# Optimization experiments

Measured on AMD Instinct MI355X. Metric: run time of the kernel, lower is better.

## Reference

```python
import jax, jax.numpy as jnp
import numpy as np

NUM_HEADS = 16

def setup_inputs() -> dict:
    key = jax.random.key(0)
    k1, k2, k3 = jax.random.split(key, 3)
    B, S, H = 2, 2048, 1024
    x = jax.random.normal(k1, (B, S, H), dtype=jnp.float32)
    w_qkv = jax.random.normal(k2, (H, 3 * H), dtype=jnp.float32) * (1.0 / np.sqrt(H))
    w_out = jax.random.normal(k3, (H, H), dtype=jnp.float32) * (1.0 / np.sqrt(H))
    return {"x": x, "w_qkv": w_qkv, "w_out": w_out}

def reference(x, w_qkv, w_out):
    B, S, H = x.shape
    nh = NUM_HEADS
    dh = H // nh
    qkv = x @ w_qkv  # (B, S, 3H)
    q, k, v = jnp.split(qkv, 3, axis=-1)
    # (B, nh, S, dh)
    q = q.reshape(B, S, nh, dh).transpose(0, 2, 1, 3)
    k = k.reshape(B, S, nh, dh).transpose(0, 2, 1, 3)
    v = v.reshape(B, S, nh, dh).transpose(0, 2, 1, 3)
    att = jnp.einsum('bhsd,bhSd->bhsS', q, k) / np.sqrt(dh).astype(np.float32)
    causal = jnp.tril(jnp.ones((S, S), dtype=bool))
    att = jnp.where(causal[None, None], att, -jnp.inf)
    att = jax.nn.softmax(att, axis=-1)
    out = jnp.einsum('bhsS,bhSd->bhsd', att, v)
    out = out.transpose(0, 2, 1, 3).reshape(B, S, H)
    return out @ w_out
```

## Files before the change

### kernel.cpp

```cpp
#include <hip/hip_runtime.h>

#define DEVINL __device__ __forceinline__

typedef __attribute__((ext_vector_type(8)))  __bf16         bf16x8;
typedef __attribute__((ext_vector_type(4)))  float          f32x4;
typedef __attribute__((ext_vector_type(16))) float          f32x16;
typedef __attribute__((ext_vector_type(8)))  unsigned short ushort8;
typedef __attribute__((ext_vector_type(4)))  unsigned short ushort4v;
typedef __attribute__((ext_vector_type(4)))  unsigned int   uint4v;
typedef __attribute__((ext_vector_type(4)))  float          float4v;

DEVINL unsigned short f2bf(float f) {
  unsigned int u = __float_as_uint(f);
  u += 0x7fffu + ((u >> 16) & 1u);
  return (unsigned short)(u >> 16);
}

DEVINL bf16x8 ldbf8(const unsigned short* p) {
  return __builtin_bit_cast(bf16x8, *(const ushort8*)p);
}

DEVINL unsigned cvtpk_bf16(float lo, float hi) {
  unsigned r;
  asm("v_cvt_pk_bf16_f32 %0, %1, %2" : "=v"(r) : "v"(lo), "v"(hi));
  return r;
}

DEVINL void gload_lds16(const unsigned short* g, unsigned short* l) {
  __builtin_amdgcn_global_load_lds((const __attribute__((address_space(1))) void*)g,
                                   (__attribute__((address_space(3))) void*)l, 16, 0, 0);
}

__global__ __launch_bounds__(256) void cvt_f32_bf16_kernel(
    const float* __restrict__ in, unsigned short* __restrict__ out, int n4) {
  int i = blockIdx.x * 256 + threadIdx.x;
  const int stride = gridDim.x * 256;
  for (; i < n4; i += stride) {
    float4v v = *(const float4v*)(in + (size_t)4 * i);
    ushort4v o;
    o[0] = f2bf(v[0]); o[1] = f2bf(v[1]); o[2] = f2bf(v[2]); o[3] = f2bf(v[3]);
    *(ushort4v*)(out + (size_t)4 * i) = o;
  }
}

__global__ __launch_bounds__(256) void transpose_cvt_kernel(
    const float* __restrict__ in, unsigned short* __restrict__ out, int R, int C) {
  __shared__ float tile[32][33];
  const int tx = threadIdx.x & 31, ty = threadIdx.x >> 5;
  const int r0 = blockIdx.y << 5, c0 = blockIdx.x << 5;
#pragma unroll
  for (int i = 0; i < 32; i += 8)
    tile[ty + i][tx] = in[(size_t)(r0 + ty + i) * C + (c0 + tx)];
  __syncthreads();
#pragma unroll
  for (int i = 0; i < 32; i += 8)
    out[(size_t)(c0 + ty + i) * R + (r0 + tx)] = f2bf(tile[tx][ty + i]);
}

__global__ __launch_bounds__(256) void v_transpose_kernel(
    const unsigned short* __restrict__ qkv, unsigned short* __restrict__ VtG) {
  const int S = 2048, LD = 3072;
  const int s0 = blockIdx.x << 5;
  const int bh = blockIdx.y;
  const int b = bh >> 4, h = bh & 15;
  __shared__ __align__(16) unsigned short T[32][72];
  const int t = threadIdx.x;
  {
    const int s = t >> 3, d0 = (t & 7) << 3;
    *(ushort8*)&T[s][d0] =
        *(const ushort8*)(qkv + ((size_t)(b * S) + s0 + s) * LD + 2048 + h * 64 + d0);
  }
  __syncthreads();
  {
    const int d = t >> 2, sc = (t & 3) << 3;
    ushort8 o;
#pragma unroll
    for (int e = 0; e < 8; ++e) o[e] = T[sc + e][d];
    *(ushort8*)(VtG + ((size_t)bh * 64 + d) * S + s0 + sc) = o;
  }
}

template <bool OUT_BF16>
__global__ __launch_bounds__(256, 3) void gemm_bt_kernel(
    const unsigned short* __restrict__ A,
    const unsigned short* __restrict__ Bt,
    void* __restrict__ Cout,
    int M, int N, int K, int lda, int ldb, int ldc) {
  __shared__ __align__(16) unsigned short As[2][128 * 32];
  __shared__ __align__(16) unsigned short Bs[2][128 * 32];
  const int tid = threadIdx.x;
  const int lane = tid & 63, wave = tid >> 6;
  const int wr = wave >> 1, wc = wave & 1;
  const int g = lane >> 4, q = lane & 15;
  const int row0 = blockIdx.x << 7, col0 = blockIdx.y << 7;

  const int srow = tid >> 2;
  const int sg = ((tid & 3) ^ (srow & 3)) << 3;
  const unsigned short* Ap0 = A + (size_t)(row0 + srow) * lda + sg;
  const unsigned short* Ap1 = Ap0 + (size_t)64 * lda;
  const unsigned short* Bp0 = Bt + (size_t)(col0 + srow) * ldb + sg;
  const unsigned short* Bp1 = Bp0 + (size_t)64 * ldb;

  f32x4 acc[4][4] = {};

  gload_lds16(Ap0, &As[0][wave * 512]);
  gload_lds16(Ap1, &As[0][2048 + wave * 512]);
  gload_lds16(Bp0, &Bs[0][wave * 512]);
  gload_lds16(Bp1, &Bs[0][2048 + wave * 512]);

  const int gx = (g ^ (q & 3)) << 3;
  const int nk = K >> 5;
  int cur = 0;

  for (int t = 0; t < nk; ++t) {
    if (t + 1 < nk) {
      Ap0 += 32; Ap1 += 32; Bp0 += 32; Bp1 += 32;
      gload_lds16(Ap0, &As[cur ^ 1][wave * 512]);
      gload_lds16(Ap1, &As[cur ^ 1][2048 + wave * 512]);
      gload_lds16(Bp0, &Bs[cur ^ 1][wave * 512]);
      gload_lds16(Bp1, &Bs[cur ^ 1][2048 + wave * 512]);
      asm volatile("s_waitcnt vmcnt(4)" ::: "memory");
    } else {
      asm volatile("s_waitcnt vmcnt(0)" ::: "memory");
    }
    __builtin_amdgcn_s_barrier();

    bf16x8 af[4], bfr[4];
#pragma unroll
    for (int mb = 0; mb < 4; ++mb)
      af[mb] = ldbf8(&As[cur][(wr * 64 + mb * 16 + q) * 32] + gx);
#pragma unroll
    for (int nb = 0; nb < 4; ++nb)
      bfr[nb] = ldbf8(&Bs[cur][(wc * 64 + nb * 16 + q) * 32] + gx);
#pragma unroll
    for (int mb = 0; mb < 4; ++mb)
#pragma unroll
      for (int nb = 0; nb < 4; ++nb)
        acc[mb][nb] = __builtin_amdgcn_mfma_f32_16x16x32_bf16(af[mb], bfr[nb], acc[mb][nb], 0, 0, 0);

    __builtin_amdgcn_s_barrier();
    cur ^= 1;
  }

#pragma unroll
  for (int mb = 0; mb < 4; ++mb)
#pragma unroll
    for (int nb = 0; nb < 4; ++nb)
#pragma unroll
      for (int r = 0; r < 4; ++r) {
        const int row = row0 + wr * 64 + mb * 16 + g * 4 + r;
        const int col = col0 + wc * 64 + nb * 16 + q;
        const float v = acc[mb][nb][r];
        if (OUT_BF16) ((unsigned short*)Cout)[(size_t)row * ldc + col] = f2bf(v);
        else          ((float*)Cout)[(size_t)row * ldc + col] = v;
      }
}

__global__ __launch_bounds__(256, 2) void attn_kernel(
    const unsigned short* __restrict__ qkv,
    const unsigned short* __restrict__ VtG,
    unsigned short* __restrict__ O) {
  const int S = 2048, H = 1024, LD = 3072;
  const int wave = threadIdx.x >> 6, lane = threadIdx.x & 63;
  const int c = lane & 31, hh = lane >> 5;

  const int L = blockIdx.x;
  const int member = L >> 8, r0_ = L & 255;
  const int pairid = r0_ & 7, bh = r0_ >> 3;
  const int qc = member ? (15 - pairid) : pairid;
  const int b = bh >> 4, h = bh & 15;
  const int q0w = qc * 128 + wave * 32;

  const unsigned short* Qb = qkv + (size_t)b * S * LD + h * 64;
  const unsigned short* Kb = Qb + H;
  const unsigned short* Vt = VtG + (size_t)(b * 16 + h) * 64 * S;

  __shared__ __align__(16) unsigned short Ks[2][64 * 64];
  __shared__ __align__(16) unsigned short Vs[2][64 * 64];

  const int srow = lane >> 3;
  const int srcg = ((lane & 7) ^ srow) << 3;
  const int wrow = wave * 8 + srow;

  gload_lds16(Kb + (size_t)wrow * LD + srcg,        Ks[0] + wave * 512);
  gload_lds16(Kb + (size_t)(32 + wrow) * LD + srcg, Ks[0] + 2048 + wave * 512);
  gload_lds16(Vt + (size_t)wrow * S + srcg,         Vs[0] + wave * 512);
  gload_lds16(Vt + (size_t)(32 + wrow) * S + srcg,  Vs[0] + 2048 + wave * 512);

  bf16x8 qf[4];
#pragma unroll
  for (int kc = 0; kc < 4; ++kc)
    qf[kc] = ldbf8(Qb + (size_t)(q0w + c) * LD + kc * 16 + hh * 8);

  f32x16 acc[2] = {};
  float m_r = -1e30f, l_r = 0.f;
  const float CE = 0.125f * 1.44269504f;

  const int ntb = qc * 2 + 2;
  int cur = 0;
  const int swz = (c & 7) << 3;

  for (int t = 0; t < ntb; ++t) {
    if (t + 1 < ntb) {
      const int c1 = (t + 1) << 6;
      unsigned short* KsN = Ks[cur ^ 1];
      unsigned short* VsN = Vs[cur ^ 1];
      gload_lds16(Kb + (size_t)(c1 + wrow) * LD + srcg,      KsN + wave * 512);
      gload_lds16(Kb + (size_t)(c1 + 32 + wrow) * LD + srcg, KsN + 2048 + wave * 512);
      gload_lds16(Vt + (size_t)wrow * S + c1 + srcg,         VsN + wave * 512);
      gload_lds16(Vt + (size_t)(32 + wrow) * S + c1 + srcg,  VsN + 2048 + wave * 512);
      asm volatile("s_waitcnt vmcnt(4)" ::: "memory");
    } else {
      asm volatile("s_waitcnt vmcnt(0)" ::: "memory");
    }
    __builtin_amdgcn_s_barrier();

    const int c0 = t << 6;
    const unsigned short* KsC = Ks[cur];
    const unsigned short* VsC = Vs[cur];

    if (c0 <= q0w + 31) {
      int nv = ((q0w + 31 - c0) >> 5) + 1; if (nv > 2) nv = 2;

      bf16x8 kf[2][4];
#pragma unroll
      for (int n = 0; n < 2; ++n) if (n < nv)
#pragma unroll
        for (int kc = 0; kc < 4; ++kc)
          kf[n][kc] = ldbf8(KsC + (n * 32 + c) * 64 + ((kc * 16 + hh * 8) ^ swz));

      f32x16 st[2] = {};
#pragma unroll
      for (int n = 0; n < 2; ++n) if (n < nv)
#pragma unroll
        for (int kc = 0; kc < 4; ++kc)
          st[n] = __builtin_amdgcn_mfma_f32_32x32x16_bf16(kf[n][kc], qf[kc], st[n], 0, 0, 0);

      bf16x8 vf[2][4];
#pragma unroll
      for (int db = 0; db < 2; ++db)
#pragma unroll
        for (int kk = 0; kk < 4; ++kk) if (kk < 2 * nv)
          vf[db][kk] = ldbf8(VsC + (db * 32 + c) * 64 + ((kk * 16 + hh * 8) ^ swz));

      if (c0 + 63 > q0w) {
#pragma unroll
        for (int n = 0; n < 2; ++n) if (n < nv)
#pragma unroll
          for (int r = 0; r < 16; ++r) {
            const int kv = c0 + n * 32 + (r & 3) + 8 * (r >> 2) + 4 * hh;
            if (kv > q0w + c) st[n][r] = -1e30f;
          }
      }

      float pmax = -1e30f;
#pragma unroll
      for (int n = 0; n < 2; ++n) if (n < nv)
#pragma unroll
        for (int r = 0; r < 16; ++r) pmax = fmaxf(pmax, st[n][r]);
      if (!__all(pmax <= m_r + 64.f)) {
        pmax = fmaxf(pmax, __shfl_xor(pmax, 32));
        const float mn = fmaxf(m_r, pmax);
        const float sf = __builtin_amdgcn_exp2f((m_r - mn) * CE);
        m_r = mn; l_r *= sf;
#pragma unroll
        for (int db = 0; db < 2; ++db) acc[db] *= sf;
      }
      const float mC = m_r * CE;
#pragma unroll
      for (int n = 0; n < 2; ++n) if (n < nv)
#pragma unroll
        for (int r = 0; r < 16; ++r) {
          const float p = __builtin_amdgcn_exp2f(fmaf(st[n][r], CE, -mC));
          st[n][r] = p;
          l_r += p;
        }

      bf16x8 pa[4];
#pragma unroll
      for (int n = 0; n < 2; ++n) if (n < nv) {
        unsigned T0 = cvtpk_bf16(st[n][0],  st[n][1]);
        unsigned T1 = cvtpk_bf16(st[n][2],  st[n][3]);
        unsigned T2 = cvtpk_bf16(st[n][4],  st[n][5]);
        unsigned T3 = cvtpk_bf16(st[n][6],  st[n][7]);
        unsigned T4 = cvtpk_bf16(st[n][8],  st[n][9]);
        unsigned T5 = cvtpk_bf16(st[n][10], st[n][11]);
        unsigned T6 = cvtpk_bf16(st[n][12], st[n][13]);
        unsigned T7 = cvtpk_bf16(st[n][14], st[n][15]);
        asm("v_permlane32_swap_b32 %0, %1" : "+v"(T0), "+v"(T2));
        asm("v_permlane32_swap_b32 %0, %1" : "+v"(T1), "+v"(T3));
        asm("v_permlane32_swap_b32 %0, %1" : "+v"(T4), "+v"(T6));
        asm("v_permlane32_swap_b32 %0, %1" : "+v"(T5), "+v"(T7));
        uint4v w0; w0[0] = T0; w0[1] = T1; w0[2] = T2; w0[3] = T3;
        uint4v w1; w1[0] = T4; w1[1] = T5; w1[2] = T6; w1[3] = T7;
        pa[2 * n]     = __builtin_bit_cast(bf16x8, w0);
        pa[2 * n + 1] = __builtin_bit_cast(bf16x8, w1);
      }

#pragma unroll
      for (int kk = 0; kk < 4; ++kk) if (kk < 2 * nv)
#pragma unroll
        for (int db = 0; db < 2; ++db)
          acc[db] = __builtin_amdgcn_mfma_f32_32x32x16_bf16(vf[db][kk], pa[kk], acc[db], 0, 0, 0);
    }

    __builtin_amdgcn_s_barrier();
    cur ^= 1;
  }

  const float lt = l_r + __shfl_xor(l_r, 32);
  const float inv = 1.f / lt;
  const size_t rowbase = (size_t)(b * S + q0w + c) * H + h * 64;
#pragma unroll
  for (int db = 0; db < 2; ++db)
#pragma unroll
    for (int blk = 0; blk < 4; ++blk) {
      ushort4v o;
#pragma unroll
      for (int j = 0; j < 4; ++j) o[j] = f2bf(acc[db][blk * 4 + j] * inv);
      *(ushort4v*)(O + rowbase + db * 32 + blk * 8 + hh * 4) = o;
    }
}

extern "C" void kernel_launch(void* const* d_in, const int* in_sizes, int n_in,
                              void* d_out, int out_size, void* d_ws, size_t ws_size,
                              hipStream_t stream) {
  const float* x     = (const float*)d_in[0];
  const float* w_qkv = (const float*)d_in[1];
  const float* w_out = (const float*)d_in[2];
  const int B = 2, S = 2048, H = 1024;
  const int M = B * S;

  unsigned short* xb    = (unsigned short*)d_ws;
  unsigned short* wqkvT = xb + (size_t)M * H;
  unsigned short* woutT = wqkvT + (size_t)3 * H * H;
  unsigned short* qkvb  = woutT + (size_t)H * H;
  unsigned short* Ob    = qkvb + (size_t)M * 3 * H;
  unsigned short* VtG   = xb;

  cvt_f32_bf16_kernel<<<1024, 256, 0, stream>>>(x, xb, (M * H) / 4);
  transpose_cvt_kernel<<<dim3((3 * H) / 32, H / 32), 256, 0, stream>>>(w_qkv, wqkvT, H, 3 * H);
  transpose_cvt_kernel<<<dim3(H / 32, H / 32), 256, 0, stream>>>(w_out, woutT, H, H);

  gemm_bt_kernel<true><<<dim3(M / 128, (3 * H) / 128), 256, 0, stream>>>(
      xb, wqkvT, qkvb, M, 3 * H, H, H, H, 3 * H);

  v_transpose_kernel<<<dim3(S / 32, 32), 256, 0, stream>>>(qkvb, VtG);

  attn_kernel<<<512, 256, 0, stream>>>(qkvb, VtG, Ob);

  gemm_bt_kernel<false><<<dim3(M / 128, H / 128), 256, 0, stream>>>(
      Ob, woutT, d_out, M, H, H, H, H, H);
}
```

Baseline: 131.2 us.

## Split attention KV range across two wave groups and fuse V transpose into GEMM

The attention kernel now uses 512 threads, with two halves of four waves each processing disjoint halves of the causal KV range for the same query rows. The halves are merged through LDS using a log-sum-exp rescale, which roughly halves the serial KV loop per block. The QKV GEMM epilogue writes V directly in transposed layout, so the separate V transpose kernel is dropped, and the QK buffer stride shrinks to 2048. s_setprio is placed around the MFMA sections. The strided transposed V stores in the GEMM epilogue are uncoalesced, and the larger blocks with a merge step add LDS traffic and synchronization.

```diff
diff --git a/kernel.cpp b/kernel.cpp
--- a/kernel.cpp
+++ b/kernel.cpp
@@ -57,35 +57,13 @@
     out[(size_t)(c0 + ty + i) * R + (r0 + tx)] = f2bf(tile[tx][ty + i]);
 }
 
-__global__ __launch_bounds__(256) void v_transpose_kernel(
-    const unsigned short* __restrict__ qkv, unsigned short* __restrict__ VtG) {
-  const int S = 2048, LD = 3072;
-  const int s0 = blockIdx.x << 5;
-  const int bh = blockIdx.y;
-  const int b = bh >> 4, h = bh & 15;
-  __shared__ __align__(16) unsigned short T[32][72];
-  const int t = threadIdx.x;
-  {
-    const int s = t >> 3, d0 = (t & 7) << 3;
-    *(ushort8*)&T[s][d0] =
-        *(const ushort8*)(qkv + ((size_t)(b * S) + s0 + s) * LD + 2048 + h * 64 + d0);
-  }
-  __syncthreads();
-  {
-    const int d = t >> 2, sc = (t & 3) << 3;
-    ushort8 o;
-#pragma unroll
-    for (int e = 0; e < 8; ++e) o[e] = T[sc + e][d];
-    *(ushort8*)(VtG + ((size_t)bh * 64 + d) * S + s0 + sc) = o;
-  }
-}
-
 template <bool OUT_BF16>
 __global__ __launch_bounds__(256, 3) void gemm_bt_kernel(
     const unsigned short* __restrict__ A,
     const unsigned short* __restrict__ Bt,
     void* __restrict__ Cout,
-    int M, int N, int K, int lda, int ldb, int ldc) {
+    int M, int N, int K, int lda, int ldb, int ldc,
+    unsigned short* __restrict__ VtOut) {
   __shared__ __align__(16) unsigned short As[2][128 * 32];
   __shared__ __align__(16) unsigned short Bs[2][128 * 32];
   const int tid = threadIdx.x;
@@ -142,6 +120,7 @@
     cur ^= 1;
   }
 
+  const bool isV = OUT_BF16 && (VtOut != nullptr) && (col0 >= 2048);
 #pragma unroll
   for (int mb = 0; mb < 4; ++mb)
 #pragma unroll
@@ -151,17 +130,25 @@
         const int row = row0 + wr * 64 + mb * 16 + g * 4 + r;
         const int col = col0 + wc * 64 + nb * 16 + q;
         const float v = acc[mb][nb][r];
-        if (OUT_BF16) ((unsigned short*)Cout)[(size_t)row * ldc + col] = f2bf(v);
-        else          ((float*)Cout)[(size_t)row * ldc + col] = v;
-      }
-}
-
-__global__ __launch_bounds__(256, 2) void attn_kernel(
+        if (isV) {
+          const int cp = col - 2048, hI = cp >> 6, dI = cp & 63;
+          VtOut[((size_t)((row >> 11) * 16 + hI) * 64 + dI) * 2048 + (row & 2047)] = f2bf(v);
+        } else if (OUT_BF16) {
+          ((unsigned short*)Cout)[(size_t)row * ldc + col] = f2bf(v);
+        } else {
+          ((float*)Cout)[(size_t)row * ldc + col] = v;
+        }
+      }
+}
+
+__global__ __launch_bounds__(512, 4) void attn_kernel(
     const unsigned short* __restrict__ qkv,
     const unsigned short* __restrict__ VtG,
     unsigned short* __restrict__ O) {
-  const int S = 2048, H = 1024, LD = 3072;
-  const int wave = threadIdx.x >> 6, lane = threadIdx.x & 63;
+  const int S = 2048, H = 1024, LD = 2048;
+  const int tid = threadIdx.x;
+  const int wave = tid >> 6, lane = tid & 63;
+  const int half = wave >> 2, wsub = wave & 3;
   const int c = lane & 31, hh = lane >> 5;
 
   const int L = blockIdx.x;
@@ -169,23 +156,30 @@
   const int pairid = r0_ & 7, bh = r0_ >> 3;
   const int qc = member ? (15 - pairid) : pairid;
   const int b = bh >> 4, h = bh & 15;
-  const int q0w = qc * 128 + wave * 32;
+  const int q0w = qc * 128 + wsub * 32;
 
   const unsigned short* Qb = qkv + (size_t)b * S * LD + h * 64;
-  const unsigned short* Kb = Qb + H;
+  const unsigned short* Kb = Qb + 1024;
   const unsigned short* Vt = VtG + (size_t)(b * 16 + h) * 64 * S;
 
-  __shared__ __align__(16) unsigned short Ks[2][64 * 64];
-  __shared__ __align__(16) unsigned short Vs[2][64 * 64];
+  __shared__ __align__(16) unsigned short smem[2][2][2][64 * 64];
+  unsigned short* Ksb = &smem[half][0][0][0];
+  unsigned short* Vsb = &smem[half][1][0][0];
 
   const int srow = lane >> 3;
   const int srcg = ((lane & 7) ^ srow) << 3;
-  const int wrow = wave * 8 + srow;
-
-  gload_lds16(Kb + (size_t)wrow * LD + srcg,        Ks[0] + wave * 512);
-  gload_lds16(Kb + (size_t)(32 + wrow) * LD + srcg, Ks[0] + 2048 + wave * 512);
-  gload_lds16(Vt + (size_t)wrow * S + srcg,         Vs[0] + wave * 512);
-  gload_lds16(Vt + (size_t)(32 + wrow) * S + srcg,  Vs[0] + 2048 + wave * 512);
+  const int wrow = wsub * 8 + srow;
+
+  const int nit = qc + 1;
+  const int tb = half ? nit : 0;
+
+  {
+    const int cc = tb << 6;
+    gload_lds16(Kb + (size_t)(cc + wrow) * LD + srcg,      Ksb + wsub * 512);
+    gload_lds16(Kb + (size_t)(cc + 32 + wrow) * LD + srcg, Ksb + 2048 + wsub * 512);
+    gload_lds16(Vt + (size_t)wrow * S + cc + srcg,         Vsb + wsub * 512);
+    gload_lds16(Vt + (size_t)(32 + wrow) * S + cc + srcg,  Vsb + 2048 + wsub * 512);
+  }
 
   bf16x8 qf[4];
 #pragma unroll
@@ -196,30 +190,29 @@
   float m_r = -1e30f, l_r = 0.f;
   const float CE = 0.125f * 1.44269504f;
 
-  const int ntb = qc * 2 + 2;
   int cur = 0;
   const int swz = (c & 7) << 3;
 
-  for (int t = 0; t < ntb; ++t) {
-    if (t + 1 < ntb) {
-      const int c1 = (t + 1) << 6;
-      unsigned short* KsN = Ks[cur ^ 1];
-      unsigned short* VsN = Vs[cur ^ 1];
-      gload_lds16(Kb + (size_t)(c1 + wrow) * LD + srcg,      KsN + wave * 512);
-      gload_lds16(Kb + (size_t)(c1 + 32 + wrow) * LD + srcg, KsN + 2048 + wave * 512);
-      gload_lds16(Vt + (size_t)wrow * S + c1 + srcg,         VsN + wave * 512);
-      gload_lds16(Vt + (size_t)(32 + wrow) * S + c1 + srcg,  VsN + 2048 + wave * 512);
+  for (int t = 0; t < nit; ++t) {
+    if (t + 1 < nit) {
+      const int c1 = (tb + t + 1) << 6;
+      unsigned short* KsN = Ksb + (cur ^ 1) * 4096;
+      unsigned short* VsN = Vsb + (cur ^ 1) * 4096;
+      gload_lds16(Kb + (size_t)(c1 + wrow) * LD + srcg,      KsN + wsub * 512);
+      gload_lds16(Kb + (size_t)(c1 + 32 + wrow) * LD + srcg, KsN + 2048 + wsub * 512);
+      gload_lds16(Vt + (size_t)wrow * S + c1 + srcg,         VsN + wsub * 512);
+      gload_lds16(Vt + (size_t)(32 + wrow) * S + c1 + srcg,  VsN + 2048 + wsub * 512);
       asm volatile("s_waitcnt vmcnt(4)" ::: "memory");
     } else {
       asm volatile("s_waitcnt vmcnt(0)" ::: "memory");
     }
     __builtin_amdgcn_s_barrier();
 
-    const int c0 = t << 6;
-    const unsigned short* KsC = Ks[cur];
-    const unsigned short* VsC = Vs[cur];
-
-    if (c0 <= q0w + 31) {
+    const int c0 = (tb + t) << 6;
+    const unsigned short* KsC = Ksb + cur * 4096;
+    const unsigned short* VsC = Vsb + cur * 4096;
+
+    if (half == 0 || c0 <= q0w + 31) {
       int nv = ((q0w + 31 - c0) >> 5) + 1; if (nv > 2) nv = 2;
 
       bf16x8 kf[2][4];
@@ -230,11 +223,13 @@
           kf[n][kc] = ldbf8(KsC + (n * 32 + c) * 64 + ((kc * 16 + hh * 8) ^ swz));
 
       f32x16 st[2] = {};
+      __builtin_amdgcn_s_setprio(1);
 #pragma unroll
       for (int n = 0; n < 2; ++n) if (n < nv)
 #pragma unroll
         for (int kc = 0; kc < 4; ++kc)
           st[n] = __builtin_amdgcn_mfma_f32_32x32x16_bf16(kf[n][kc], qf[kc], st[n], 0, 0, 0);
+      __builtin_amdgcn_s_setprio(0);
 
       bf16x8 vf[2][4];
 #pragma unroll
@@ -297,11 +292,13 @@
         pa[2 * n + 1] = __builtin_bit_cast(bf16x8, w1);
       }
 
+      __builtin_amdgcn_s_setprio(1);
 #pragma unroll
       for (int kk = 0; kk < 4; ++kk) if (kk < 2 * nv)
 #pragma unroll
         for (int db = 0; db < 2; ++db)
           acc[db] = __builtin_amdgcn_mfma_f32_32x32x16_bf16(vf[db][kk], pa[kk], acc[db], 0, 0, 0);
+      __builtin_amdgcn_s_setprio(0);
     }
 
     __builtin_amdgcn_s_barrier();
@@ -309,17 +306,36 @@
   }
 
   const float lt = l_r + __shfl_xor(l_r, 32);
-  const float inv = 1.f / lt;
-  const size_t rowbase = (size_t)(b * S + q0w + c) * H + h * 64;
-#pragma unroll
-  for (int db = 0; db < 2; ++db)
-#pragma unroll
-    for (int blk = 0; blk < 4; ++blk) {
-      ushort4v o;
-#pragma unroll
-      for (int j = 0; j < 4; ++j) o[j] = f2bf(acc[db][blk * 4 + j] * inv);
-      *(ushort4v*)(O + rowbase + db * 32 + blk * 8 + hh * 4) = o;
-    }
+  __syncthreads();
+  float* mrg = (float*)&smem[0][0][0][0];
+  if (half) {
+    float* p = mrg + (wsub * 64 + lane) * 36;
+#pragma unroll
+    for (int j = 0; j < 16; ++j) { p[j] = acc[0][j]; p[16 + j] = acc[1][j]; }
+    p[32] = m_r; p[33] = lt;
+  }
+  __syncthreads();
+  if (!half) {
+    const float* p = mrg + (wsub * 64 + lane) * 36;
+    const float mh = p[32], lth = p[33];
+    const float mn = fmaxf(m_r, mh);
+    const float sfl = __builtin_amdgcn_exp2f((m_r - mn) * CE);
+    const float sfh = __builtin_amdgcn_exp2f((mh - mn) * CE);
+    const float inv = 1.f / (lt * sfl + lth * sfh);
+    const size_t rowbase = (size_t)(b * S + q0w + c) * H + h * 64;
+#pragma unroll
+    for (int db = 0; db < 2; ++db)
+#pragma unroll
+      for (int blk = 0; blk < 4; ++blk) {
+        ushort4v o;
+#pragma unroll
+        for (int j = 0; j < 4; ++j) {
+          const int idx = blk * 4 + j;
+          o[j] = f2bf((acc[db][idx] * sfl + p[db * 16 + idx] * sfh) * inv);
+        }
+        *(ushort4v*)(O + rowbase + db * 32 + blk * 8 + hh * 4) = o;
+      }
+  }
 }
 
 extern "C" void kernel_launch(void* const* d_in, const int* in_sizes, int n_in,
@@ -334,21 +350,19 @@
   unsigned short* xb    = (unsigned short*)d_ws;
   unsigned short* wqkvT = xb + (size_t)M * H;
   unsigned short* woutT = wqkvT + (size_t)3 * H * H;
-  unsigned short* qkvb  = woutT + (size_t)H * H;
-  unsigned short* Ob    = qkvb + (size_t)M * 3 * H;
-  unsigned short* VtG   = xb;
+  unsigned short* qkb   = woutT + (size_t)H * H;
+  unsigned short* VtG   = qkb + (size_t)M * 2048;
+  unsigned short* Ob    = VtG + (size_t)B * 16 * 64 * S;
 
   cvt_f32_bf16_kernel<<<1024, 256, 0, stream>>>(x, xb, (M * H) / 4);
   transpose_cvt_kernel<<<dim3((3 * H) / 32, H / 32), 256, 0, stream>>>(w_qkv, wqkvT, H, 3 * H);
   transpose_cvt_kernel<<<dim3(H / 32, H / 32), 256, 0, stream>>>(w_out, woutT, H, H);
 
   gemm_bt_kernel<true><<<dim3(M / 128, (3 * H) / 128), 256, 0, stream>>>(
-      xb, wqkvT, qkvb, M, 3 * H, H, H, H, 3 * H);
-
-  v_transpose_kernel<<<dim3(S / 32, 32), 256, 0, stream>>>(qkvb, VtG);
-
-  attn_kernel<<<512, 256, 0, stream>>>(qkvb, VtG, Ob);
+      xb, wqkvT, qkb, M, 3 * H, H, H, H, 2048, VtG);
+
+  attn_kernel<<<512, 512, 0, stream>>>(qkb, VtG, Ob);
 
   gemm_bt_kernel<false><<<dim3(M / 128, H / 128), 256, 0, stream>>>(
-      Ob, woutT, d_out, M, H, H, H, H, H);
-}
+      Ob, woutT, d_out, M, H, H, H, H, H, nullptr);
+}
```

Measured after the change: 262.5 us. 2x slower.
